# Performance work log

Measured on AMD Instinct MI355X. Metric: run time of the kernel, lower is better.

## Reference

```python
import jax, jax.numpy as jnp
import numpy as np

B, T = 4, 16000
V = 256      # input_channels (token vocab)
R = 256      # residual_channels
S = 512      # skip_channels
O = 256      # output_channels
L = 16       # layers
DIL = 256    # 2 ** (floor(log2(max_dilation=128)) + 1) -- same for every layer (as in source)


def setup_inputs() -> dict:
    key = jax.random.key(0)
    ks = jax.random.split(key, 12)
    tokens = jax.random.randint(ks[0], (B, T), 0, V)
    embed = jax.random.normal(ks[1], (V, R), jnp.float32) * 0.05
    dilate_w = jax.random.normal(ks[2], (L, 2 * R, R, 2), jnp.float32) * 0.05
    dilate_b = jax.random.normal(ks[3], (L, 2 * R), jnp.float32) * 0.01
    res_w = jax.random.normal(ks[4], (L - 1, R, R), jnp.float32) * 0.05
    res_b = jax.random.normal(ks[5], (L - 1, R), jnp.float32) * 0.01
    skip_w = jax.random.normal(ks[6], (L, S, R), jnp.float32) * 0.05
    skip_b = jax.random.normal(ks[7], (L, S), jnp.float32) * 0.01
    conv_out_w = jax.random.normal(ks[8], (O, S), jnp.float32) * 0.05
    conv_end_w = jax.random.normal(ks[9], (O, O), jnp.float32) * 0.05
    return {
        'tokens': tokens, 'embed': embed,
        'dilate_w': dilate_w, 'dilate_b': dilate_b,
        'res_w': res_w, 'res_b': res_b,
        'skip_w': skip_w, 'skip_b': skip_b,
        'conv_out_w': conv_out_w, 'conv_end_w': conv_end_w,
    }


def _wavenet(tokens, embed, dilate_w, dilate_b, res_w, res_b, skip_w, skip_b,
             conv_out_w, conv_end_w):
    x = embed[tokens]                 # [B,T,R]
    x = jnp.transpose(x, (0, 2, 1))   # [B,R,T]
    skip = None
    for l in range(L):
        # causal dilated conv, kernel=2: y[t] = W0 @ x[t-DIL] + W1 @ x[t] + b
        x_shift = jnp.pad(x, ((0, 0), (0, 0), (DIL, 0)))[:, :, :T]
        in_act = (jnp.einsum('oi,bit->bot', dilate_w[l, :, :, 0], x_shift)
                  + jnp.einsum('oi,bit->bot', dilate_w[l, :, :, 1], x)
                  + dilate_b[l][None, :, None])      # [B,2R,T]
        g = in_act[:, :R, :]                          # source uses SAME slice for tanh & sigmoid
        act = jnp.tanh(g) * jax.nn.sigmoid(g)         # [B,R,T]
        if l < L - 1:
            res = jnp.einsum('oi,bit->bot', res_w[l], act) + res_b[l][None, :, None]
            x = res + x
        s = jnp.einsum('si,bit->bst', skip_w[l], act) + skip_b[l][None, :, None]
        skip = s if skip is None else skip + s
    out = jax.nn.relu(skip)
    out = jnp.einsum('os,bst->bot', conv_out_w, out)
    out = jax.nn.relu(out)
    out = jnp.einsum('po,bot->bpt', conv_end_w, out)
    return jax.nn.softmax(out, axis=1)                # softmax over channel dim


def reference(tokens, embed, dilate_w, dilate_b, res_w, res_b, skip_w, skip_b,
              conv_out_w, conv_end_w):
    return _wavenet(tokens, embed, dilate_w, dilate_b, res_w, res_b,
                    skip_w, skip_b, conv_out_w, conv_end_w)
```

## Files before the change

kernel.cpp:

```cpp
#include <hip/hip_runtime.h>
#include <hip/hip_fp16.h>

#define TLEN 16000

typedef _Float16 h16;
typedef __attribute__((ext_vector_type(8))) _Float16 half8;
typedef __attribute__((ext_vector_type(4))) _Float16 half4;
typedef __attribute__((ext_vector_type(4))) float f32x4;

__device__ __forceinline__ void gload16(const void* g, void* l) {
  __builtin_amdgcn_global_load_lds((const __attribute__((address_space(1))) void*)g,
                                   (__attribute__((address_space(3))) void*)l, 16, 0, 0);
}

__device__ __forceinline__ float gated_act(float g) {
  float gc = fmaxf(g, -30.0f);
  float e1 = __expf(-gc);
  float e2 = e1 * e1;
  return (1.0f - e2) / ((1.0f + e2) * (1.0f + e1));
}

__global__ __launch_bounds__(256) void prep_k(
    const float* __restrict__ dw, const float* __restrict__ rw,
    const float* __restrict__ sw, const float* __restrict__ cow,
    const float* __restrict__ cew, const float* __restrict__ sb,
    h16* __restrict__ w2h, h16* __restrict__ resh, h16* __restrict__ skiph,
    h16* __restrict__ couth, h16* __restrict__ cendh, float* __restrict__ sbias,
    h16* __restrict__ x16p)
{
  size_t u = (size_t)blockIdx.x * 256 + threadIdx.x;
  if (u < 2097152) {
    int l = (int)(u >> 17);
    int rem = (int)(u & 131071);
    int o = rem >> 9, k = rem & 511;
    float v = (k < 256) ? dw[(((size_t)l * 512 + o) * 256 + k) * 2]
                        : dw[(((size_t)l * 512 + o) * 256 + (k - 256)) * 2 + 1];
    w2h[u] = (h16)v;
    return;
  }
  u -= 2097152;
  if (u < 983040) { resh[u] = (h16)rw[u]; return; }
  u -= 983040;
  if (u < 2097152) {
    int s = (int)(u >> 12);
    int r = (int)(u & 4095);
    int l = r >> 8, c = r & 255;
    skiph[u] = (h16)sw[((size_t)l * 512 + s) * 256 + c];
    return;
  }
  u -= 2097152;
  if (u < 131072) { couth[u] = (h16)cow[u]; return; }
  u -= 131072;
  if (u < 65536) { cendh[u] = (h16)cew[u]; return; }
  u -= 65536;
  if (u < 512) {
    float s = 0.f;
    for (int l = 0; l < 16; l++) s += sb[(size_t)l * 512 + u];
    sbias[u] = s;
    return;
  }
  u -= 512;
  if (u < 65536) x16p[u] = (h16)0.f;
}

__global__ __launch_bounds__(256) void embed_k(
    const int* __restrict__ tok, const float* __restrict__ emb,
    float* __restrict__ x, h16* __restrict__ x16p)
{
  const size_t i = (size_t)blockIdx.x * 256 + threadIdx.x;
  const int t = (int)(i >> 6);
  const int c4 = (int)(i & 63) * 4;
  const int tk = tok[t];
  f32x4 v = *(const f32x4*)(emb + (size_t)tk * 256 + c4);
  *(f32x4*)(x + (size_t)t * 256 + c4) = v;
  half4 hv;
#pragma unroll
  for (int j = 0; j < 4; j++) hv[j] = (h16)v[j];
  *(half4*)(x16p + (size_t)(t + 256) * 256 + c4) = hv;
}

template<int KTOT, int AST, int WST, int BN, int MODE>
__global__ __launch_bounds__(256) void gemm4_k(
    const h16* __restrict__ A, const h16* __restrict__ W,
    const float* __restrict__ bias, h16* __restrict__ o16,
    float* __restrict__ of32, const float* __restrict__ sp_in)
{
  constexpr int NT = KTOT / 32;
  constexpr int MI = (BN == 128) ? 2 : 4;
  constexpr int OST = (MODE == 0) ? 2048 : (MODE == 3) ? 512 : 256;
  __shared__ h16 As[2][64 * 32];
  __shared__ h16 Bs[2][BN * 32];
  __shared__ __align__(16) char tscr[17408];
  h16 (*tbufH)[16][72] = (h16(*)[16][72])tscr;
  float (*tbufF)[16][68] = (float(*)[16][68])tscr;

  const int tid  = threadIdx.x;
  const int lane = tid & 63;
  const int w    = tid >> 6;
  const int r16  = lane & 15;
  const int kg   = lane >> 4;
  const int t0   = blockIdx.x * 64;
  const int n0w  = blockIdx.y * BN;
  const int wm   = (BN == 128) ? (w >> 1) : 0;
  const int wn   = (BN == 128) ? (w & 1) : w;
  const int arow_base = wm * 32;
  const int brow_base = wn * 64;
  const int srow  = lane >> 2;
  const int sunit = (lane & 3) * 8;

  auto stage = [&](int bi, int kk) {
    const int k0 = kk * 32;
    {
      const h16* src;
      if constexpr (MODE == 0)
        src = A + (size_t)(t0 + w * 16 + srow + (k0 < 256 ? 0 : 256)) * AST + (k0 & 255) + sunit;
      else
        src = A + (size_t)(t0 + w * 16 + srow) * AST + k0 + sunit;
      gload16(src, &As[bi][(w * 16) * 32]);
    }
#pragma unroll
    for (int q = 0; q < BN / 64; q++) {
      const int row = w * (BN / 4) + q * 16;
      const h16* src = W + (size_t)(n0w + row + srow) * WST + k0 + sunit;
      gload16(src, &Bs[bi][row * 32]);
    }
  };

  f32x4 acc[MI][4];
#pragma unroll
  for (int i = 0; i < MI; i++)
#pragma unroll
    for (int j = 0; j < 4; j++) acc[i][j] = (f32x4){0.f, 0.f, 0.f, 0.f};

  stage(0, 0);
  __syncthreads();

  for (int t = 0; t < NT; t++) {
    const int cur = t & 1;
    if (t + 1 < NT) stage(cur ^ 1, t + 1);
    half8 af[MI], bf[4];
#pragma unroll
    for (int mi = 0; mi < MI; mi++)
      af[mi] = *(const half8*)&As[cur][(arow_base + mi * 16 + r16) * 32 + kg * 8];
#pragma unroll
    for (int ni = 0; ni < 4; ni++)
      bf[ni] = *(const half8*)&Bs[cur][(brow_base + ni * 16 + r16) * 32 + kg * 8];
#pragma unroll
    for (int mi = 0; mi < MI; mi++)
#pragma unroll
      for (int ni = 0; ni < 4; ni++)
        acc[mi][ni] = __builtin_amdgcn_mfma_f32_16x16x32_f16(af[mi], bf[ni], acc[mi][ni], 0, 0, 0);
    __syncthreads();
  }

  const int rr = lane >> 2;
  const int cc = (lane & 3) * 16;
  const int colw = n0w + brow_base;

#pragma unroll
  for (int mi = 0; mi < MI; mi++) {
    const int trow = t0 + arow_base + mi * 16;
    if constexpr (MODE == 1 || MODE == 2 || MODE == 3) {
#pragma unroll
      for (int ni = 0; ni < 4; ni++)
#pragma unroll
        for (int g = 0; g < 4; g++) {
          float v = acc[mi][ni][g];
          if constexpr (MODE == 1) v += bias[colw + ni * 16 + r16];
          tbufF[w][kg * 4 + g][ni * 16 + r16] = v;
        }
      if constexpr (MODE == 1) {
        float* xrow = of32 + (size_t)(trow + rr) * 256 + colw + cc;
        h16* xprow = o16 + (size_t)(trow + rr + 256) * 256 + colw + cc;
        half8 hv0, hv1;
#pragma unroll
        for (int j = 0; j < 4; j++) {
          f32x4 v = *(const f32x4*)(xrow + j * 4);
          f32x4 d = *(const f32x4*)&tbufF[w][rr][cc + j * 4];
          v += d;
          *(f32x4*)(xrow + j * 4) = v;
#pragma unroll
          for (int e = 0; e < 4; e++) {
            if (j < 2) hv0[j * 4 + e] = (h16)v[e];
            else       hv1[(j - 2) * 4 + e] = (h16)v[e];
          }
        }
        *(half8*)xprow       = hv0;
        *(half8*)(xprow + 8) = hv1;
      } else if constexpr (MODE == 2) {
        float* dst = of32 + (size_t)(trow + rr) * 512 + colw + cc;
#pragma unroll
        for (int j = 0; j < 4; j++)
          *(f32x4*)(dst + j * 4) = *(const f32x4*)&tbufF[w][rr][cc + j * 4];
      } else {
        const float* sprow = sp_in + (size_t)(trow + rr) * 512 + colw + cc;
        h16* dst = o16 + (size_t)(trow + rr) * 512 + colw + cc;
        half8 hv0, hv1;
#pragma unroll
        for (int j = 0; j < 4; j++) {
          f32x4 v = *(const f32x4*)&tbufF[w][rr][cc + j * 4];
          f32x4 s = *(const f32x4*)(sprow + j * 4);
          f32x4 sb = *(const f32x4*)(bias + colw + cc + j * 4);
          v = v + s + sb;
#pragma unroll
          for (int e = 0; e < 4; e++) {
            float r = fmaxf(v[e], 0.f);
            if (j < 2) hv0[j * 4 + e] = (h16)r;
            else       hv1[(j - 2) * 4 + e] = (h16)r;
          }
        }
        *(half8*)dst       = hv0;
        *(half8*)(dst + 8) = hv1;
      }
    } else {
#pragma unroll
      for (int ni = 0; ni < 4; ni++)
#pragma unroll
        for (int g = 0; g < 4; g++) {
          float v = acc[mi][ni][g];
          if constexpr (MODE == 0) v = gated_act(v + bias[colw + ni * 16 + r16]);
          else                     v = fmaxf(v, 0.f);
          tbufH[w][kg * 4 + g][ni * 16 + r16] = (h16)v;
        }
      h16* dst = o16 + (size_t)(trow + rr) * OST + colw + cc;
      *(half8*)dst       = *(const half8*)&tbufH[w][rr][cc];
      *(half8*)(dst + 8) = *(const half8*)&tbufH[w][rr][cc + 8];
    }
  }
}

__global__ __launch_bounds__(256) void head_k(
    const h16* __restrict__ A, const h16* __restrict__ W, float* __restrict__ out)
{
  __shared__ h16 As[32][40];
  __shared__ h16 Bs[256][40];
  __shared__ float lg[32][257];

  const int tid = threadIdx.x;
  const int t0  = blockIdx.x * 32;
  const int lane = tid & 63, wid = tid >> 6;
  const int r16 = lane & 15, kg = lane >> 4;

  f32x4 acc[2][4];
#pragma unroll
  for (int i = 0; i < 2; i++)
#pragma unroll
    for (int j = 0; j < 4; j++) acc[i][j] = (f32x4){0.f, 0.f, 0.f, 0.f};

  const int arow = tid >> 3, asub = tid & 7;

  for (int k0 = 0; k0 < 256; k0 += 32) {
    {
      const h16* src = A + (size_t)(t0 + arow) * 256 + k0 + asub * 4;
      *(half4*)&As[arow][asub * 4] = *(const half4*)src;
    }
    {
      const h16* src = W + (size_t)tid * 256 + k0;
#pragma unroll
      for (int q = 0; q < 4; q++) *(half8*)&Bs[tid][q * 8] = *(const half8*)(src + q * 8);
    }
    __syncthreads();
    half8 af[2], bf[4];
#pragma unroll
    for (int mi = 0; mi < 2; mi++) af[mi] = *(const half8*)&As[mi * 16 + r16][kg * 8];
#pragma unroll
    for (int ni = 0; ni < 4; ni++) bf[ni] = *(const half8*)&Bs[wid * 64 + ni * 16 + r16][kg * 8];
#pragma unroll
    for (int mi = 0; mi < 2; mi++)
#pragma unroll
      for (int ni = 0; ni < 4; ni++)
        acc[mi][ni] = __builtin_amdgcn_mfma_f32_16x16x32_f16(af[mi], bf[ni], acc[mi][ni], 0, 0, 0);
    __syncthreads();
  }

#pragma unroll
  for (int mi = 0; mi < 2; mi++) {
    const int rl = mi * 16 + kg * 4;
#pragma unroll
    for (int ni = 0; ni < 4; ni++) {
      const int n = wid * 64 + ni * 16 + r16;
#pragma unroll
      for (int g = 0; g < 4; g++) lg[rl + g][n] = acc[mi][ni][g];
    }
  }
  __syncthreads();

  for (int i = 0; i < 8; i++) {
    const int r = wid * 8 + i;
    float v[4];
#pragma unroll
    for (int j = 0; j < 4; j++) v[j] = lg[r][lane + 64 * j];
    float m = fmaxf(fmaxf(v[0], v[1]), fmaxf(v[2], v[3]));
#pragma unroll
    for (int off = 32; off >= 1; off >>= 1) m = fmaxf(m, __shfl_xor(m, off));
    float s = 0.f;
#pragma unroll
    for (int j = 0; j < 4; j++) { v[j] = __expf(v[j] - m); s += v[j]; }
#pragma unroll
    for (int off = 32; off >= 1; off >>= 1) s += __shfl_xor(s, off);
    const float inv = 1.f / s;
#pragma unroll
    for (int j = 0; j < 4; j++) lg[r][lane + 64 * j] = v[j] * inv;
  }
  __syncthreads();

  const int tl = tid & 31, og = tid >> 5;
  for (int j = 0; j < 32; j++) {
    const int o = og * 32 + j;
    out[(size_t)o * TLEN + t0 + tl] = lg[tl][o];
  }
}

extern "C" void kernel_launch(void* const* d_in, const int* in_sizes, int n_in,
                              void* d_out, int out_size, void* d_ws, size_t ws_size,
                              hipStream_t stream)
{
  const int*   tokens = (const int*)  d_in[0];
  const float* embedw = (const float*)d_in[1];
  const float* dil_w  = (const float*)d_in[2];
  const float* dil_b  = (const float*)d_in[3];
  const float* resw   = (const float*)d_in[4];
  const float* resb   = (const float*)d_in[5];
  const float* skipw  = (const float*)d_in[6];
  const float* skipb  = (const float*)d_in[7];
  const float* coutw  = (const float*)d_in[8];
  const float* cendw  = (const float*)d_in[9];
  float* out = (float*)d_out;

  char* p = (char*)d_ws;
  auto carve = [&](size_t bytes) { char* r = p; p += (bytes + 255) & ~(size_t)255; return r; };
  h16* w2h      = (h16*)carve((size_t)16 * 256 * 512 * 2);
  h16* resh     = (h16*)carve((size_t)15 * 256 * 256 * 2);
  h16* skiph    = (h16*)carve((size_t)512 * 4096 * 2);
  h16* couth    = (h16*)carve((size_t)256 * 512 * 2);
  h16* cendh    = (h16*)carve((size_t)256 * 256 * 2);
  float* sbias  = (float*)carve(512 * 4);
  float* xf32   = (float*)carve((size_t)TLEN * 256 * 4);
  h16*  x16p    = (h16*) carve((size_t)(TLEN + 256) * 256 * 2);
  h16*  act     = (h16*) carve((size_t)TLEN * 2048 * 2);
  float* sp     = (float*)carve((size_t)TLEN * 512 * 4);
  h16* sk16 = (h16*)xf32;
  h16* h116 = act;

  prep_k<<<dim3(21250), 256, 0, stream>>>(
      dil_w, resw, skipw, coutw, cendw, skipb,
      w2h, resh, skiph, couth, cendh, sbias, x16p);

  for (int b = 0; b < 4; b++) {
    embed_k<<<dim3(4000), 256, 0, stream>>>(tokens + (size_t)b * TLEN, embedw, xf32, x16p);

    for (int l = 0; l < 16; l++) {
      gemm4_k<512, 256, 512, 128, 0><<<dim3(250, 2), 256, 0, stream>>>(
          x16p, w2h + (size_t)l * 131072, dil_b + (size_t)l * 512,
          act + (l & 7) * 256, nullptr, nullptr);
      if (l < 15)
        gemm4_k<256, 2048, 256, 128, 1><<<dim3(250, 2), 256, 0, stream>>>(
            act + (l & 7) * 256, resh + (size_t)l * 65536, resb + (size_t)l * 256,
            x16p, xf32, nullptr);
      if (l == 7)
        gemm4_k<2048, 2048, 4096, 256, 2><<<dim3(250, 2), 256, 0, stream>>>(
            act, skiph, nullptr, nullptr, sp, nullptr);
    }

    gemm4_k<2048, 2048, 4096, 256, 3><<<dim3(250, 2), 256, 0, stream>>>(
        act, skiph + 2048, sbias, sk16, nullptr, sp);
    gemm4_k<512, 512, 512, 128, 4><<<dim3(250, 2), 256, 0, stream>>>(
        sk16, couth, nullptr, h116, nullptr, nullptr);
    head_k<<<dim3(500), 256, 0, stream>>>(h116, cendh, out + (size_t)b * 256 * TLEN);
  }
}
```

Measured before the change: 2.714 ms.

## Batch two sequences per launch and fuse fp32-to-fp16 conversion into dilated GEMM

Launches now cover two batch items at a time through a z grid dimension, doubling the blocks per launch (500 to 1000) and halving the number of launches. The dilated-conv GEMM reads the fp32 residual directly and converts it to fp16 in registers, with the causal shift applied in the index math. This removes the padded fp16 copy of x and its extra write. The skip GEMM is split into four chunks of four layers with fp16 partial sums, which shrinks the activation buffer, and launch bounds now request higher occupancy. In exchange, the skip partials lose precision in fp16 and the A operand no longer goes through async LDS loads.

```diff
diff --git a/kernel.cpp b/kernel.cpp
--- a/kernel.cpp
+++ b/kernel.cpp
@@ -2,6 +2,7 @@
 #include <hip/hip_fp16.h>
 
 #define TLEN 16000
+#define BC 2
 
 typedef _Float16 h16;
 typedef __attribute__((ext_vector_type(8))) _Float16 half8;
@@ -25,8 +26,7 @@
     const float* __restrict__ sw, const float* __restrict__ cow,
     const float* __restrict__ cew, const float* __restrict__ sb,
     h16* __restrict__ w2h, h16* __restrict__ resh, h16* __restrict__ skiph,
-    h16* __restrict__ couth, h16* __restrict__ cendh, float* __restrict__ sbias,
-    h16* __restrict__ x16p)
+    h16* __restrict__ couth, h16* __restrict__ cendh, float* __restrict__ sbias)
 {
   size_t u = (size_t)blockIdx.x * 256 + threadIdx.x;
   if (u < 2097152) {
@@ -42,9 +42,11 @@
   if (u < 983040) { resh[u] = (h16)rw[u]; return; }
   u -= 983040;
   if (u < 2097152) {
-    int s = (int)(u >> 12);
-    int r = (int)(u & 4095);
-    int l = r >> 8, c = r & 255;
+    int ch = (int)(u >> 19);
+    int r  = (int)(u & 524287);
+    int s  = r >> 10;
+    int q  = r & 1023;
+    int l  = ch * 4 + (q >> 8), c = q & 255;
     skiph[u] = (h16)sw[((size_t)l * 512 + s) * 256 + c];
     return;
   }
@@ -57,162 +59,122 @@
     float s = 0.f;
     for (int l = 0; l < 16; l++) s += sb[(size_t)l * 512 + u];
     sbias[u] = s;
-    return;
-  }
-  u -= 512;
-  if (u < 65536) x16p[u] = (h16)0.f;
+  }
 }
 
 __global__ __launch_bounds__(256) void embed_k(
-    const int* __restrict__ tok, const float* __restrict__ emb,
-    float* __restrict__ x, h16* __restrict__ x16p)
-{
+    const int* __restrict__ tok, const float* __restrict__ emb, float* __restrict__ x)
+{
+  const int b = blockIdx.y;
   const size_t i = (size_t)blockIdx.x * 256 + threadIdx.x;
   const int t = (int)(i >> 6);
   const int c4 = (int)(i & 63) * 4;
-  const int tk = tok[t];
-  f32x4 v = *(const f32x4*)(emb + (size_t)tk * 256 + c4);
-  *(f32x4*)(x + (size_t)t * 256 + c4) = v;
-  half4 hv;
-#pragma unroll
-  for (int j = 0; j < 4; j++) hv[j] = (h16)v[j];
-  *(half4*)(x16p + (size_t)(t + 256) * 256 + c4) = hv;
-}
-
-template<int KTOT, int AST, int WST, int BN, int MODE>
-__global__ __launch_bounds__(256) void gemm4_k(
-    const h16* __restrict__ A, const h16* __restrict__ W,
+  const int tk = tok[(size_t)b * TLEN + t];
+  *(f32x4*)(x + ((size_t)b * TLEN + t) * 256 + c4) = *(const f32x4*)(emb + (size_t)tk * 256 + c4);
+}
+
+template<int KTOT, int AST, int WST, int MODE>
+__global__ __launch_bounds__(256, 4) void gemm5_k(
+    const void* __restrict__ A, const h16* __restrict__ W,
     const float* __restrict__ bias, h16* __restrict__ o16,
-    float* __restrict__ of32, const float* __restrict__ sp_in)
+    float* __restrict__ of32, const h16* __restrict__ spin)
 {
   constexpr int NT = KTOT / 32;
-  constexpr int MI = (BN == 128) ? 2 : 4;
-  constexpr int OST = (MODE == 0) ? 2048 : (MODE == 3) ? 512 : 256;
-  __shared__ h16 As[2][64 * 32];
-  __shared__ h16 Bs[2][BN * 32];
-  __shared__ __align__(16) char tscr[17408];
-  h16 (*tbufH)[16][72] = (h16(*)[16][72])tscr;
-  float (*tbufF)[16][68] = (float(*)[16][68])tscr;
+  __shared__ __align__(16) char smem[24576];
+  h16* As = (h16*)smem;
+  h16* Bs = (h16*)smem + 4096;
 
   const int tid  = threadIdx.x;
   const int lane = tid & 63;
   const int w    = tid >> 6;
   const int r16  = lane & 15;
   const int kg   = lane >> 4;
+  const int wm   = w >> 1;
+  const int wn   = w & 1;
   const int t0   = blockIdx.x * 64;
-  const int n0w  = blockIdx.y * BN;
-  const int wm   = (BN == 128) ? (w >> 1) : 0;
-  const int wn   = (BN == 128) ? (w & 1) : w;
-  const int arow_base = wm * 32;
-  const int brow_base = wn * 64;
-  const int srow  = lane >> 2;
-  const int sunit = (lane & 3) * 8;
-
-  auto stage = [&](int bi, int kk) {
-    const int k0 = kk * 32;
-    {
-      const h16* src;
-      if constexpr (MODE == 0)
-        src = A + (size_t)(t0 + w * 16 + srow + (k0 < 256 ? 0 : 256)) * AST + (k0 & 255) + sunit;
-      else
-        src = A + (size_t)(t0 + w * 16 + srow) * AST + k0 + sunit;
-      gload16(src, &As[bi][(w * 16) * 32]);
-    }
-#pragma unroll
-    for (int q = 0; q < BN / 64; q++) {
-      const int row = w * (BN / 4) + q * 16;
-      const h16* src = W + (size_t)(n0w + row + srow) * WST + k0 + sunit;
-      gload16(src, &Bs[bi][row * 32]);
+  const int n0w  = blockIdx.y * 128;
+  const int bz   = blockIdx.z;
+  const int srow = lane >> 2;
+  const int sc8  = (lane & 3) * 8;
+
+  const float* Af = (const float*)A + (size_t)bz * TLEN * 256;
+  const h16*   Ah = (const h16*)A + (size_t)bz * TLEN * (size_t)AST;
+
+  auto stageB = [&](int bi, int k0) {
+#pragma unroll
+    for (int q = 0; q < 2; q++) {
+      const h16* src = W + (size_t)(n0w + w * 32 + q * 16 + srow) * WST + k0 + sc8;
+      gload16(src, Bs + bi * 4096 + (w * 32 + q * 16) * 32);
     }
   };
-
-  f32x4 acc[MI][4];
-#pragma unroll
-  for (int i = 0; i < MI; i++)
+  auto stageA = [&](int bi, int k0) {
+    const h16* src = Ah + (size_t)(t0 + w * 16 + srow) * AST + k0 + sc8;
+    gload16(src, As + bi * 2048 + (w * 16) * 32);
+  };
+  auto loadA0 = [&](int k0) -> half8 {
+    half8 av;
+#pragma unroll
+    for (int j = 0; j < 8; j++) av[j] = (h16)0.f;
+    const bool tap0 = (k0 < 256);
+    if (!(tap0 && t0 < 256)) {
+      const int srcrow = t0 + w * 16 + srow - (tap0 ? 256 : 0);
+      const float* s = Af + (size_t)srcrow * 256 + (k0 & 255) + sc8;
+      f32x4 v0 = *(const f32x4*)s;
+      f32x4 v1 = *(const f32x4*)(s + 4);
+#pragma unroll
+      for (int j = 0; j < 4; j++) { av[j] = (h16)v0[j]; av[j + 4] = (h16)v1[j]; }
+    }
+    return av;
+  };
+
+  f32x4 acc[2][4];
+#pragma unroll
+  for (int i = 0; i < 2; i++)
 #pragma unroll
     for (int j = 0; j < 4; j++) acc[i][j] = (f32x4){0.f, 0.f, 0.f, 0.f};
 
-  stage(0, 0);
+  half8 areg;
+  if constexpr (MODE == 0) areg = loadA0(0);
+  stageB(0, 0);
+  if constexpr (MODE != 0) stageA(0, 0);
+  else *(half8*)(As + (w * 16 + srow) * 32 + sc8) = areg;
   __syncthreads();
 
   for (int t = 0; t < NT; t++) {
     const int cur = t & 1;
-    if (t + 1 < NT) stage(cur ^ 1, t + 1);
-    half8 af[MI], bf[4];
-#pragma unroll
-    for (int mi = 0; mi < MI; mi++)
-      af[mi] = *(const half8*)&As[cur][(arow_base + mi * 16 + r16) * 32 + kg * 8];
+    if (t + 1 < NT) {
+      if constexpr (MODE == 0) areg = loadA0((t + 1) * 32);
+      stageB(cur ^ 1, (t + 1) * 32);
+      if constexpr (MODE != 0) stageA(cur ^ 1, (t + 1) * 32);
+    }
+    half8 af[2], bf[4];
+#pragma unroll
+    for (int mi = 0; mi < 2; mi++)
+      af[mi] = *(const half8*)&As[cur * 2048 + (wm * 32 + mi * 16 + r16) * 32 + kg * 8];
 #pragma unroll
     for (int ni = 0; ni < 4; ni++)
-      bf[ni] = *(const half8*)&Bs[cur][(brow_base + ni * 16 + r16) * 32 + kg * 8];
-#pragma unroll
-    for (int mi = 0; mi < MI; mi++)
+      bf[ni] = *(const half8*)&Bs[cur * 4096 + (wn * 64 + ni * 16 + r16) * 32 + kg * 8];
+#pragma unroll
+    for (int mi = 0; mi < 2; mi++)
 #pragma unroll
       for (int ni = 0; ni < 4; ni++)
         acc[mi][ni] = __builtin_amdgcn_mfma_f32_16x16x32_f16(af[mi], bf[ni], acc[mi][ni], 0, 0, 0);
+    if (t + 1 < NT)
+      if constexpr (MODE == 0)
+        *(half8*)(As + (cur ^ 1) * 2048 + (w * 16 + srow) * 32 + sc8) = areg;
     __syncthreads();
   }
 
+  h16*   tb = (h16*)(smem + w * 4352);
+  float* tf = (float*)(smem + w * 4352);
   const int rr = lane >> 2;
   const int cc = (lane & 3) * 16;
-  const int colw = n0w + brow_base;
-
-#pragma unroll
-  for (int mi = 0; mi < MI; mi++) {
-    const int trow = t0 + arow_base + mi * 16;
-    if constexpr (MODE == 1 || MODE == 2 || MODE == 3) {
-#pragma unroll
-      for (int ni = 0; ni < 4; ni++)
-#pragma unroll
-        for (int g = 0; g < 4; g++) {
-          float v = acc[mi][ni][g];
-          if constexpr (MODE == 1) v += bias[colw + ni * 16 + r16];
-          tbufF[w][kg * 4 + g][ni * 16 + r16] = v;
-        }
-      if constexpr (MODE == 1) {
-        float* xrow = of32 + (size_t)(trow + rr) * 256 + colw + cc;
-        h16* xprow = o16 + (size_t)(trow + rr + 256) * 256 + colw + cc;
-        half8 hv0, hv1;
-#pragma unroll
-        for (int j = 0; j < 4; j++) {
-          f32x4 v = *(const f32x4*)(xrow + j * 4);
-          f32x4 d = *(const f32x4*)&tbufF[w][rr][cc + j * 4];
-          v += d;
-          *(f32x4*)(xrow + j * 4) = v;
-#pragma unroll
-          for (int e = 0; e < 4; e++) {
-            if (j < 2) hv0[j * 4 + e] = (h16)v[e];
-            else       hv1[(j - 2) * 4 + e] = (h16)v[e];
-          }
-        }
-        *(half8*)xprow       = hv0;
-        *(half8*)(xprow + 8) = hv1;
-      } else if constexpr (MODE == 2) {
-        float* dst = of32 + (size_t)(trow + rr) * 512 + colw + cc;
-#pragma unroll
-        for (int j = 0; j < 4; j++)
-          *(f32x4*)(dst + j * 4) = *(const f32x4*)&tbufF[w][rr][cc + j * 4];
-      } else {
-        const float* sprow = sp_in + (size_t)(trow + rr) * 512 + colw + cc;
-        h16* dst = o16 + (size_t)(trow + rr) * 512 + colw + cc;
-        half8 hv0, hv1;
-#pragma unroll
-        for (int j = 0; j < 4; j++) {
-          f32x4 v = *(const f32x4*)&tbufF[w][rr][cc + j * 4];
-          f32x4 s = *(const f32x4*)(sprow + j * 4);
-          f32x4 sb = *(const f32x4*)(bias + colw + cc + j * 4);
-          v = v + s + sb;
-#pragma unroll
-          for (int e = 0; e < 4; e++) {
-            float r = fmaxf(v[e], 0.f);
-            if (j < 2) hv0[j * 4 + e] = (h16)r;
-            else       hv1[(j - 2) * 4 + e] = (h16)r;
-          }
-        }
-        *(half8*)dst       = hv0;
-        *(half8*)(dst + 8) = hv1;
-      }
-    } else {
+  const int colw = n0w + wn * 64;
+
+#pragma unroll
+  for (int mi = 0; mi < 2; mi++) {
+    const int trow = t0 + wm * 32 + mi * 16;
+    if constexpr (MODE == 0 || MODE == 5) {
 #pragma unroll
       for (int ni = 0; ni < 4; ni++)
 #pragma unroll
@@ -220,11 +182,53 @@
           float v = acc[mi][ni][g];
           if constexpr (MODE == 0) v = gated_act(v + bias[colw + ni * 16 + r16]);
           else                     v = fmaxf(v, 0.f);
-          tbufH[w][kg * 4 + g][ni * 16 + r16] = (h16)v;
+          tb[(kg * 4 + g) * 72 + ni * 16 + r16] = (h16)v;
         }
-      h16* dst = o16 + (size_t)(trow + rr) * OST + colw + cc;
-      *(half8*)dst       = *(const half8*)&tbufH[w][rr][cc];
-      *(half8*)(dst + 8) = *(const half8*)&tbufH[w][rr][cc + 8];
+      constexpr int OST = (MODE == 0) ? 1024 : 256;
+      h16* dst = o16 + (size_t)bz * TLEN * OST + (size_t)(trow + rr) * OST + colw + cc;
+      *(half8*)dst       = *(const half8*)&tb[rr * 72 + cc];
+      *(half8*)(dst + 8) = *(const half8*)&tb[rr * 72 + cc + 8];
+    } else {
+#pragma unroll
+      for (int ni = 0; ni < 4; ni++)
+#pragma unroll
+        for (int g = 0; g < 4; g++) {
+          float v = acc[mi][ni][g];
+          if constexpr (MODE == 1 || MODE == 2) v += bias[colw + ni * 16 + r16];
+          tf[(kg * 4 + g) * 68 + ni * 16 + r16] = v;
+        }
+      if constexpr (MODE == 1) {
+        float* xrow = of32 + (size_t)bz * TLEN * 256 + (size_t)(trow + rr) * 256 + colw + cc;
+#pragma unroll
+        for (int j = 0; j < 4; j++) {
+          f32x4 v = *(const f32x4*)(xrow + j * 4);
+          v += *(const f32x4*)(tf + rr * 68 + cc + j * 4);
+          *(f32x4*)(xrow + j * 4) = v;
+        }
+      } else {
+        half8 o0, o1;
+        if constexpr (MODE == 2) {
+#pragma unroll
+          for (int e = 0; e < 8; e++) {
+            o0[e] = (h16)tf[rr * 68 + cc + e];
+            o1[e] = (h16)tf[rr * 68 + cc + 8 + e];
+          }
+        } else {
+          const h16* sps = spin + (size_t)bz * TLEN * 512 + (size_t)(trow + rr) * 512 + colw + cc;
+          half8 s0 = *(const half8*)sps;
+          half8 s1 = *(const half8*)(sps + 8);
+#pragma unroll
+          for (int e = 0; e < 8; e++) {
+            float v0 = tf[rr * 68 + cc + e] + (float)s0[e];
+            float v1 = tf[rr * 68 + cc + 8 + e] + (float)s1[e];
+            if constexpr (MODE == 4) { v0 = fmaxf(v0, 0.f); v1 = fmaxf(v1, 0.f); }
+            o0[e] = (h16)v0; o1[e] = (h16)v1;
+          }
+        }
+        h16* dst = o16 + (size_t)bz * TLEN * 512 + (size_t)(trow + rr) * 512 + colw + cc;
+        *(half8*)dst       = o0;
+        *(half8*)(dst + 8) = o1;
+      }
     }
   }
 }
@@ -237,9 +241,11 @@
   __shared__ float lg[32][257];
 
   const int tid = threadIdx.x;
+  const int bz  = blockIdx.z;
   const int t0  = blockIdx.x * 32;
   const int lane = tid & 63, wid = tid >> 6;
   const int r16 = lane & 15, kg = lane >> 4;
+  const h16* Ab = A + (size_t)bz * TLEN * 256;
 
   f32x4 acc[2][4];
 #pragma unroll
@@ -251,7 +257,7 @@
 
   for (int k0 = 0; k0 < 256; k0 += 32) {
     {
-      const h16* src = A + (size_t)(t0 + arow) * 256 + k0 + asub * 4;
+      const h16* src = Ab + (size_t)(t0 + arow) * 256 + k0 + asub * 4;
       *(half4*)&As[arow][asub * 4] = *(const half4*)src;
     }
     {
@@ -307,7 +313,7 @@
   const int tl = tid & 31, og = tid >> 5;
   for (int j = 0; j < 32; j++) {
     const int o = og * 32 + j;
-    out[(size_t)o * TLEN + t0 + tl] = lg[tl][o];
+    out[((size_t)bz * 256 + o) * TLEN + t0 + tl] = lg[tl][o];
   }
 }
 
@@ -331,41 +337,47 @@
   auto carve = [&](size_t bytes) { char* r = p; p += (bytes + 255) & ~(size_t)255; return r; };
   h16* w2h      = (h16*)carve((size_t)16 * 256 * 512 * 2);
   h16* resh     = (h16*)carve((size_t)15 * 256 * 256 * 2);
-  h16* skiph    = (h16*)carve((size_t)512 * 4096 * 2);
+  h16* skiph    = (h16*)carve((size_t)4 * 512 * 1024 * 2);
   h16* couth    = (h16*)carve((size_t)256 * 512 * 2);
   h16* cendh    = (h16*)carve((size_t)256 * 256 * 2);
   float* sbias  = (float*)carve(512 * 4);
-  float* xf32   = (float*)carve((size_t)TLEN * 256 * 4);
-  h16*  x16p    = (h16*) carve((size_t)(TLEN + 256) * 256 * 2);
-  h16*  act     = (h16*) carve((size_t)TLEN * 2048 * 2);
-  float* sp     = (float*)carve((size_t)TLEN * 512 * 4);
+  float* xf32   = (float*)carve((size_t)BC * TLEN * 256 * 4);
+  h16*  act     = (h16*) carve((size_t)BC * TLEN * 1024 * 2);
+  h16*  sp      = (h16*) carve((size_t)BC * TLEN * 512 * 2);
   h16* sk16 = (h16*)xf32;
   h16* h116 = act;
 
-  prep_k<<<dim3(21250), 256, 0, stream>>>(
-      dil_w, resw, skipw, coutw, cendw, skipb,
-      w2h, resh, skiph, couth, cendh, sbias, x16p);
-
-  for (int b = 0; b < 4; b++) {
-    embed_k<<<dim3(4000), 256, 0, stream>>>(tokens + (size_t)b * TLEN, embedw, xf32, x16p);
+  prep_k<<<dim3(20994), 256, 0, stream>>>(
+      dil_w, resw, skipw, coutw, cendw, skipb, w2h, resh, skiph, couth, cendh, sbias);
+
+  for (int c0 = 0; c0 < 4; c0 += BC) {
+    embed_k<<<dim3(4000, BC), 256, 0, stream>>>(tokens + (size_t)c0 * TLEN, embedw, xf32);
 
     for (int l = 0; l < 16; l++) {
-      gemm4_k<512, 256, 512, 128, 0><<<dim3(250, 2), 256, 0, stream>>>(
-          x16p, w2h + (size_t)l * 131072, dil_b + (size_t)l * 512,
-          act + (l & 7) * 256, nullptr, nullptr);
+      gemm5_k<512, 256, 512, 0><<<dim3(250, 2, BC), 256, 0, stream>>>(
+          xf32, w2h + (size_t)l * 131072, dil_b + (size_t)l * 512,
+          act + (l & 3) * 256, nullptr, nullptr);
       if (l < 15)
-        gemm4_k<256, 2048, 256, 128, 1><<<dim3(250, 2), 256, 0, stream>>>(
-            act + (l & 7) * 256, resh + (size_t)l * 65536, resb + (size_t)l * 256,
-            x16p, xf32, nullptr);
-      if (l == 7)
-        gemm4_k<2048, 2048, 4096, 256, 2><<<dim3(250, 2), 256, 0, stream>>>(
-            act, skiph, nullptr, nullptr, sp, nullptr);
-    }
-
-    gemm4_k<2048, 2048, 4096, 256, 3><<<dim3(250, 2), 256, 0, stream>>>(
-        act, skiph + 2048, sbias, sk16, nullptr, sp);
-    gemm4_k<512, 512, 512, 128, 4><<<dim3(250, 2), 256, 0, stream>>>(
+        gemm5_k<256, 1024, 256, 1><<<dim3(250, 2, BC), 256, 0, stream>>>(
+            act + (l & 3) * 256, resh + (size_t)l * 65536, resb + (size_t)l * 256,
+            nullptr, xf32, nullptr);
+      if ((l & 3) == 3) {
+        const int ch = l >> 2;
+        const h16* Wc = skiph + (size_t)ch * 524288;
+        if (ch == 0)
+          gemm5_k<1024, 1024, 1024, 2><<<dim3(250, 4, BC), 256, 0, stream>>>(
+              act, Wc, sbias, sp, nullptr, nullptr);
+        else if (ch < 3)
+          gemm5_k<1024, 1024, 1024, 3><<<dim3(250, 4, BC), 256, 0, stream>>>(
+              act, Wc, nullptr, sp, nullptr, sp);
+        else
+          gemm5_k<1024, 1024, 1024, 4><<<dim3(250, 4, BC), 256, 0, stream>>>(
+              act, Wc, nullptr, sk16, nullptr, sp);
+      }
+    }
+
+    gemm5_k<512, 512, 512, 5><<<dim3(250, 2, BC), 256, 0, stream>>>(
         sk16, couth, nullptr, h116, nullptr, nullptr);
-    head_k<<<dim3(500), 256, 0, stream>>>(h116, cendh, out + (size_t)b * 256 * TLEN);
-  }
-}
+    head_k<<<dim3(500, 1, BC), 256, 0, stream>>>(h116, cendh, out + (size_t)c0 * 256 * TLEN);
+  }
+}
```

Result: faster. 2.281 ms (-16.0%).
